# Kernel optimization log

Measured on AMD Instinct MI355X. Metric: run time of the kernel, lower is better.

Reference implementation:

```python
import jax, jax.numpy as jnp
import numpy as np

B, T, D, V, S = 32, 512, 1024, 50257, 16
FWD_SLOTS, NUM_PAIRS, REV_SLOTS, CONF = 4, 4, 2, 0.8
LN_EPS = 1e-5


def setup_inputs() -> dict:
    key = jax.random.key(0)
    ks = jax.random.split(key, 8)
    s = 0.02
    return dict(
        seq=jax.random.randint(ks[0], (B, T), 0, V),
        embed=jax.random.normal(ks[1], (V, D), jnp.float32) * s,
        ff_w1=jax.random.normal(ks[2], (D, 2 * D), jnp.float32) * s,
        ff_b1=jnp.zeros((2 * D,), jnp.float32),
        ff_w2=jax.random.normal(ks[3], (2 * D, D), jnp.float32) * s,
        ff_b2=jnp.zeros((D,), jnp.float32),
        ln_g=jnp.ones((D,), jnp.float32),
        ln_b=jnp.zeros((D,), jnp.float32),
        wg_w=jax.random.normal(ks[4], (D, S), jnp.float32) * s,
        wg_b=jnp.zeros((S,), jnp.float32),
        rp_w=jax.random.normal(ks[5], (D, D), jnp.float32) * s,
        rp_b=jnp.zeros((D,), jnp.float32),
        out_w=jax.random.normal(ks[6], (D, V), jnp.float32) * s,
        out_b=jnp.zeros((V,), jnp.float32),
        memory=jax.random.normal(ks[7], (1, S, D), jnp.float32) * s,
    )


def reference(seq, embed, ff_w1, ff_b1, ff_w2, ff_b2, ln_g, ln_b,
              wg_w, wg_b, rp_w, rp_b, out_w, out_b, memory):
    # --- Encoder: embed -> LayerNorm(h + FFN(h)) ---
    h = embed[seq]                                           # [B,T,D]
    ff = jax.nn.relu(h @ ff_w1 + ff_b1) @ ff_w2 + ff_b2
    x = h + ff
    mu = x.mean(-1, keepdims=True)
    var = ((x - mu) ** 2).mean(-1, keepdims=True)
    hiddens = (x - mu) / jnp.sqrt(var + LN_EPS) * ln_g + ln_b

    # --- write_memory on hiddens[:, :-1, :] ---
    hw = hiddens[:, :-1, :]                                  # [B,Tw,D]
    Tw = hw.shape[1]
    slot_imp = (hw @ wg_w + wg_b).mean(-1)                   # [B,Tw]
    F_size = min(FWD_SLOTS, Tw)
    _, top_idx = jax.lax.top_k(slot_imp, F_size)             # [B,F]
    fwd_hidden = jnp.take_along_axis(hw, top_idx[..., None], axis=1)  # [B,F,D]
    mem = jnp.broadcast_to(memory, (hw.shape[0], S, hw.shape[2]))
    mem = mem.at[:, jnp.arange(F_size) % S].set(fwd_hidden)

    # retroactive writes: skipped = first min(Tw, 2*NUM_PAIRS) positions not in top_idx.
    # Since Kp - F_size >= 4 >= REV_SLOTS, n_rev is always REV_SLOTS (vectorizable).
    Kp = min(Tw, 2 * NUM_PAIRS)
    pos = jnp.arange(Kp)
    in_top = (pos[None, :, None] == top_idx[:, None, :]).any(-1)     # [B,Kp]
    masked = jnp.where(in_top, -jnp.inf, slot_imp[:, :Kp])
    _, rev_pos = jax.lax.top_k(masked, REV_SLOTS)                    # [B,2]
    rev_hidden = jnp.take_along_axis(hw, rev_pos[..., None], axis=1) # [B,2,D]
    mem = mem.at[:, (FWD_SLOTS + jnp.arange(REV_SLOTS)) % S].set(rev_hidden)

    # --- read with suppression ---
    query = hiddens[:, -1, :]                                # [B,D]
    direct_logits = query @ out_w + out_b                    # [B,V]
    conf = jax.nn.softmax(direct_logits, axis=-1).max(-1)
    use_mem = (conf < CONF).astype(query.dtype)[:, None]
    q = query @ rp_w + rp_b
    scores = jnp.einsum('bsd,bd->bs', mem, q)                # [B,S]
    attn = jax.nn.softmax(scores, axis=-1)
    ctx = jnp.einsum('bs,bsd->bd', attn, mem)
    ctx = ctx * use_mem + query * (1.0 - use_mem)
    return ctx @ out_w + out_b                               # [B,V]
```

## Files before the change

kernel.cpp:

```cpp
#include <hip/hip_runtime.h>
#include <stdint.h>
#include <math.h>

#define B_ 32
#define T_ 512
#define D_ 1024
#define H_ 2048
#define V_ 50257
#define S_ 16
#define M_ (B_*T_)
#define TW_ 511

typedef __attribute__((ext_vector_type(8))) short bf16x8;
typedef __attribute__((ext_vector_type(4))) float f32x4;
typedef __attribute__((ext_vector_type(8))) unsigned short us8;
typedef __attribute__((ext_vector_type(4))) unsigned short us4;

__device__ inline unsigned short f2bf(float f) {
  uint32_t u = __builtin_bit_cast(uint32_t, f);
  uint32_t r = (u + 0x7FFFu + ((u >> 16) & 1u)) >> 16;
  return (unsigned short)r;
}
__device__ inline float bf2f(unsigned short h) {
  uint32_t u = ((uint32_t)h) << 16;
  return __builtin_bit_cast(float, u);
}

__device__ inline f32x4 mfma_bf16(bf16x8 a, bf16x8 b, f32x4 c) {
  return __builtin_amdgcn_mfma_f32_16x16x32_bf16(a, b, c, 0, 0, 0);
}

__device__ inline void gl2lds(const unsigned short* g, unsigned short* l) {
  __builtin_amdgcn_global_load_lds(
      (const __attribute__((address_space(1))) unsigned int*)g,
      (__attribute__((address_space(3))) unsigned int*)l,
      16, 0, 0);
}

__global__ __launch_bounds__(256) void k_prep(
    const float* __restrict__ wg_w, const float* __restrict__ wg_b,
    const float* __restrict__ ln_g, const float* __restrict__ ln_b,
    const float* __restrict__ b2,
    float* __restrict__ gu, float* __restrict__ scal) {
  __shared__ float r1[4], r2[4], r3[4], r4[4];
  int tid = threadIdx.x;
  float psgu = 0.f, plbu = 0.f, pb2g = 0.f, pb2s = 0.f;
  for (int d = tid; d < D_; d += 256) {
    float s = 0.f;
    #pragma unroll
    for (int j = 0; j < S_; j++) s += wg_w[d*S_ + j];
    float uu = s * (1.0f/S_);
    float g = ln_g[d] * uu;
    gu[d] = g;
    psgu += g;
    plbu += ln_b[d] * uu;
    pb2g += b2[d] * g;
    pb2s += b2[d];
  }
  for (int off = 32; off > 0; off >>= 1) {
    psgu += __shfl_down(psgu, off, 64); plbu += __shfl_down(plbu, off, 64);
    pb2g += __shfl_down(pb2g, off, 64); pb2s += __shfl_down(pb2s, off, 64);
  }
  if ((tid & 63) == 0) { int w = tid>>6; r1[w]=psgu; r2[w]=plbu; r3[w]=pb2g; r4[w]=pb2s; }
  __syncthreads();
  if (tid == 0) {
    float sgu = r1[0]+r1[1]+r1[2]+r1[3];
    float lbu = r2[0]+r2[1]+r2[2]+r2[3];
    float ub = 0.f;
    for (int j = 0; j < S_; j++) ub += wg_b[j];
    scal[0] = sgu;
    scal[1] = lbu + ub * (1.0f/S_);
    scal[2] = r3[0]+r3[1]+r3[2]+r3[3];
    scal[3] = r4[0]+r4[1]+r4[2]+r4[3];
  }
}

__global__ __launch_bounds__(256) void k_prep2(
    const float* __restrict__ W2, const float* __restrict__ gu,
    float* __restrict__ w2gu, float* __restrict__ w2s) {
  int h = blockIdx.x*4 + (threadIdx.x >> 6);
  int lane = threadIdx.x & 63;
  const float4* row = (const float4*)(W2 + (size_t)h*D_);
  const float4* g4 = (const float4*)gu;
  float sg = 0.f, ss = 0.f;
  #pragma unroll
  for (int k = 0; k < 4; k++) {
    float4 w = row[lane + k*64];
    float4 g = g4[lane + k*64];
    sg += w.x*g.x + w.y*g.y + w.z*g.z + w.w*g.w;
    ss += w.x + w.y + w.z + w.w;
  }
  for (int off = 32; off > 0; off >>= 1) { sg += __shfl_down(sg, off, 64); ss += __shfl_down(ss, off, 64); }
  if (lane == 0) { w2gu[h] = sg; w2s[h] = ss; }
}

__global__ __launch_bounds__(256) void k_gsplit(
    const int* __restrict__ seq, const float* __restrict__ embed,
    const float* __restrict__ gu,
    unsigned short* __restrict__ ehi, unsigned short* __restrict__ elo,
    float* __restrict__ es, float* __restrict__ egu) {
  int m = blockIdx.x;
  int tok = seq[m];
  int tid = threadIdx.x;
  int d = tid * 4;
  float4 v = *(const float4*)(embed + (size_t)tok*D_ + d);
  float4 g = *(const float4*)(gu + d);
  unsigned short h0=f2bf(v.x), h1=f2bf(v.y), h2=f2bf(v.z), h3=f2bf(v.w);
  us4 hv = {h0,h1,h2,h3};
  us4 lv = {f2bf(v.x-bf2f(h0)), f2bf(v.y-bf2f(h1)), f2bf(v.z-bf2f(h2)), f2bf(v.w-bf2f(h3))};
  *(us4*)(ehi + (size_t)m*D_ + d) = hv;
  *(us4*)(elo + (size_t)m*D_ + d) = lv;
  float pe = v.x + v.y + v.z + v.w;
  float pg = v.x*g.x + v.y*g.y + v.z*g.z + v.w*g.w;
  __shared__ float le[4], lg[4];
  for (int off = 32; off > 0; off >>= 1) { pe += __shfl_down(pe, off, 64); pg += __shfl_down(pg, off, 64); }
  if ((tid & 63) == 0) { le[tid>>6] = pe; lg[tid>>6] = pg; }
  __syncthreads();
  if (tid == 0) {
    es[m]  = le[0]+le[1]+le[2]+le[3];
    egu[m] = lg[0]+lg[1]+lg[2]+lg[3];
  }
}

__global__ __launch_bounds__(256) void k_tsplit(
    const float* __restrict__ W, unsigned short* __restrict__ Thi,
    unsigned short* __restrict__ Tlo, int K, int N) {
  __shared__ float tile[32][33];
  int k0 = blockIdx.x * 32, n0 = blockIdx.y * 32;
  int tx = threadIdx.x & 31, ty = threadIdx.x >> 5;
  for (int i = ty; i < 32; i += 8)
    tile[i][tx] = W[(size_t)(k0+i)*N + n0 + tx];
  __syncthreads();
  for (int i = ty; i < 32; i += 8) {
    float v = tile[tx][i];
    unsigned short hi = f2bf(v);
    size_t o = (size_t)(n0+i)*K + k0 + tx;
    Thi[o] = hi;
    if (Tlo) Tlo[o] = f2bf(v - bf2f(hi));
  }
}

__global__ __launch_bounds__(256) void k_gemm1(
    const unsigned short* __restrict__ ehi, const unsigned short* __restrict__ elo,
    const unsigned short* __restrict__ Bhi, const unsigned short* __restrict__ Blo,
    const float* __restrict__ b1,
    const float* __restrict__ w2gu, const float* __restrict__ w2s,
    unsigned short* __restrict__ rhi,
    float* __restrict__ rg, float* __restrict__ rsum) {
  __shared__ unsigned short Ah[128*32], Al[128*32], Bh[128*32], Bl[128*32];
  int m0 = blockIdx.x * 128, n0 = blockIdx.y * 128;
  int tid = threadIdx.x;
  int lane = tid & 63, wave = tid >> 6;
  int wm = (wave & 1) * 64, wn = (wave >> 1) * 64;
  int fr = lane & 15, fq = lane >> 4;
  int srow = lane >> 2;
  int scol = ((lane & 3) ^ ((lane >> 3) & 3)) * 8;
  int csw = (fq ^ ((fr >> 1) & 3)) * 8;

  f32x4 acc[4][4];
  #pragma unroll
  for (int i=0;i<4;i++)
    #pragma unroll
    for (int j=0;j<4;j++) acc[i][j] = (f32x4){0.f,0.f,0.f,0.f};

  const unsigned short *pAh[2], *pAl[2], *pBh[2], *pBl[2];
  unsigned short *lAh[2], *lAl[2], *lBh[2], *lBl[2];
  #pragma unroll
  for (int t = 0; t < 2; t++) {
    int rb = t*64 + wave*16;
    pAh[t] = ehi + (size_t)(m0 + rb + srow)*D_ + scol;
    pAl[t] = elo + (size_t)(m0 + rb + srow)*D_ + scol;
    pBh[t] = Bhi + (size_t)(n0 + rb + srow)*D_ + scol;
    pBl[t] = Blo + (size_t)(n0 + rb + srow)*D_ + scol;
    lAh[t] = &Ah[rb*32]; lAl[t] = &Al[rb*32];
    lBh[t] = &Bh[rb*32]; lBl[t] = &Bl[rb*32];
  }

  for (int k0 = 0; k0 < D_; k0 += 32) {
    #pragma unroll
    for (int t = 0; t < 2; t++) {
      gl2lds(pAh[t], lAh[t]); gl2lds(pAl[t], lAl[t]);
      gl2lds(pBh[t], lBh[t]); gl2lds(pBl[t], lBl[t]);
      pAh[t] += 32; pAl[t] += 32; pBh[t] += 32; pBl[t] += 32;
    }
    __syncthreads();

    bf16x8 ah[4], al[4], bh[4], bl[4];
    #pragma unroll
    for (int i=0;i<4;i++) {
      ah[i] = *(const bf16x8*)&Ah[(wm + i*16 + fr)*32 + csw];
      al[i] = *(const bf16x8*)&Al[(wm + i*16 + fr)*32 + csw];
      bh[i] = *(const bf16x8*)&Bh[(wn + i*16 + fr)*32 + csw];
      bl[i] = *(const bf16x8*)&Bl[(wn + i*16 + fr)*32 + csw];
    }
    #pragma unroll
    for (int i=0;i<4;i++)
      #pragma unroll
      for (int j=0;j<4;j++) {
        acc[i][j] = mfma_bf16(ah[i], bh[j], acc[i][j]);
        acc[i][j] = mfma_bf16(ah[i], bl[j], acc[i][j]);
        acc[i][j] = mfma_bf16(al[i], bh[j], acc[i][j]);
      }
    __syncthreads();
  }

  float biasj[4], wgj[4], wsj[4];
  int gcj[4];
  #pragma unroll
  for (int j=0;j<4;j++) {
    gcj[j] = n0 + wn + j*16 + fr;
    biasj[j] = b1[gcj[j]];
    wgj[j] = w2gu[gcj[j]];
    wsj[j] = w2s[gcj[j]];
  }
  #pragma unroll
  for (int i=0;i<4;i++) {
    #pragma unroll
    for (int r=0;r<4;r++) {
      int gr = m0 + wm + i*16 + fq*4 + r;
      float sg = 0.f, ss = 0.f;
      #pragma unroll
      for (int j=0;j<4;j++) {
        float v = acc[i][j][r] + biasj[j];
        v = fmaxf(v, 0.f);
        rhi[(size_t)gr*H_ + gcj[j]] = f2bf(v);
        sg += v * wgj[j];
        ss += v * wsj[j];
      }
      #pragma unroll
      for (int off = 8; off > 0; off >>= 1) {
        sg += __shfl_down(sg, off, 16);
        ss += __shfl_down(ss, off, 16);
      }
      if (fr == 0) {
        atomicAdd(&rg[gr], sg);
        atomicAdd(&rsum[gr], ss);
      }
    }
  }
}

__global__ __launch_bounds__(256) void k_gemm2(
    const unsigned short* __restrict__ Ahi, const unsigned short* __restrict__ Bhig,
    const float* __restrict__ b2, const int* __restrict__ seq,
    const float* __restrict__ embed, float* __restrict__ xout) {
  __shared__ unsigned short Ah[128*32], Bh[128*32];
  int m0 = blockIdx.x * 128, n0 = blockIdx.y * 128;
  int tid = threadIdx.x;
  int lane = tid & 63, wave = tid >> 6;
  int wm = (wave & 1) * 64, wn = (wave >> 1) * 64;
  int fr = lane & 15, fq = lane >> 4;
  int srow = lane >> 2;
  int scol = ((lane & 3) ^ ((lane >> 3) & 3)) * 8;
  int csw = (fq ^ ((fr >> 1) & 3)) * 8;

  f32x4 acc[4][4];
  #pragma unroll
  for (int i=0;i<4;i++)
    #pragma unroll
    for (int j=0;j<4;j++) acc[i][j] = (f32x4){0.f,0.f,0.f,0.f};

  const unsigned short *pA[2], *pB[2];
  unsigned short *lA[2], *lB[2];
  #pragma unroll
  for (int t = 0; t < 2; t++) {
    int rb = t*64 + wave*16;
    pA[t] = Ahi  + (size_t)(m0 + rb + srow)*H_ + scol;
    pB[t] = Bhig + (size_t)(n0 + rb + srow)*H_ + scol;
    lA[t] = &Ah[rb*32]; lB[t] = &Bh[rb*32];
  }

  for (int k0 = 0; k0 < H_; k0 += 32) {
    #pragma unroll
    for (int t = 0; t < 2; t++) {
      gl2lds(pA[t], lA[t]); gl2lds(pB[t], lB[t]);
      pA[t] += 32; pB[t] += 32;
    }
    __syncthreads();

    bf16x8 ah[4], bh[4];
    #pragma unroll
    for (int i=0;i<4;i++) {
      ah[i] = *(const bf16x8*)&Ah[(wm + i*16 + fr)*32 + csw];
      bh[i] = *(const bf16x8*)&Bh[(wn + i*16 + fr)*32 + csw];
    }
    #pragma unroll
    for (int i=0;i<4;i++)
      #pragma unroll
      for (int j=0;j<4;j++)
        acc[i][j] = mfma_bf16(ah[i], bh[j], acc[i][j]);
    __syncthreads();
  }

  #pragma unroll
  for (int j=0;j<4;j++) {
    int gc = n0 + wn + j*16 + fr;
    float bias = b2[gc];
    #pragma unroll
    for (int i=0;i<4;i++) {
      #pragma unroll
      for (int r=0;r<4;r++) {
        int gr = m0 + wm + i*16 + fq*4 + r;
        float h = embed[(size_t)seq[gr]*D_ + gc];
        xout[(size_t)gr*D_ + gc] = acc[i][j][r] + bias + h;
      }
    }
  }
}

__global__ __launch_bounds__(256) void k_stats(
    const float* __restrict__ x, const float* __restrict__ scal,
    const float* __restrict__ es, const float* __restrict__ egu,
    const float* __restrict__ rg, const float* __restrict__ rsum,
    float* __restrict__ meanv, float* __restrict__ rstdv, float* __restrict__ slotv) {
  int m = blockIdx.x, tid = threadIdx.x;
  const float4* xr = (const float4*)(x + (size_t)m*D_);
  float4 v = xr[tid];
  float sq = v.x*v.x + v.y*v.y + v.z*v.z + v.w*v.w;
  __shared__ float lq[4];
  for (int off = 32; off > 0; off >>= 1) sq += __shfl_down(sq, off, 64);
  if ((tid & 63) == 0) lq[tid>>6] = sq;
  __syncthreads();
  if (tid == 0) {
    sq = lq[0]+lq[1]+lq[2]+lq[3];
    float mu = (es[m] + rsum[m] + scal[3]) * (1.0f/D_);
    float sg = egu[m] + rg[m] + scal[2];
    float var = sq * (1.0f/D_) - mu*mu;
    float rs = 1.0f / sqrtf(var + 1e-5f);
    meanv[m] = mu; rstdv[m] = rs;
    slotv[m] = rs * (sg - mu * scal[0]) + scal[1];
  }
}

__global__ __launch_bounds__(256) void k_select(const float* __restrict__ slotv, int* __restrict__ sel) {
  __shared__ float v[TW_];
  __shared__ float bvs[4]; __shared__ int bis[4];
  int b = blockIdx.x, tid = threadIdx.x;
  for (int t = tid; t < TW_; t += 256) v[t] = slotv[(size_t)b*T_ + t];
  __syncthreads();
  for (int k = 0; k < 4; k++) {
    float bv = -3.4e38f; int bi = 0x7fffffff;
    for (int t = tid; t < TW_; t += 256) {
      float x = v[t];
      if (x > bv) { bv = x; bi = t; }
    }
    for (int off = 32; off > 0; off >>= 1) {
      float ov = __shfl_down(bv, off, 64); int oi = __shfl_down(bi, off, 64);
      if (ov > bv || (ov == bv && oi < bi)) { bv = ov; bi = oi; }
    }
    if ((tid & 63) == 0) { bvs[tid>>6] = bv; bis[tid>>6] = bi; }
    __syncthreads();
    if (tid == 0) {
      float fbv = bvs[0]; int fbi = bis[0];
      for (int w = 1; w < 4; w++)
        if (bvs[w] > fbv || (bvs[w] == fbv && bis[w] < fbi)) { fbv = bvs[w]; fbi = bis[w]; }
      sel[b*8 + k] = fbi; v[fbi] = -3.4e38f;
    }
    __syncthreads();
  }
  if (tid == 0) {
    for (int k = 4; k < 6; k++) {
      float best = -3.4e38f; int bi = 0;
      for (int t = 0; t < 8; t++) if (v[t] > best) { best = v[t]; bi = t; }
      sel[b*8 + k] = bi; v[bi] = -3.4e38f;
    }
  }
}

__global__ __launch_bounds__(256) void k_buildmem(
    const float* __restrict__ x, const float* __restrict__ meanv, const float* __restrict__ rstdv,
    const float* __restrict__ ln_g, const float* __restrict__ ln_b,
    const float* __restrict__ memory, const int* __restrict__ sel,
    float* __restrict__ mem, float* __restrict__ qv) {
  int s = blockIdx.x, b = blockIdx.y, tid = threadIdx.x;
  int d = tid * 4;
  if (s >= 6 && s < 16) {
    *(float4*)&mem[((size_t)b*S_ + s)*D_ + d] = *(const float4*)&memory[(size_t)s*D_ + d];
    return;
  }
  int t = (s == 16) ? (T_ - 1) : sel[b*8 + s];
  int m = b*T_ + t;
  float mu = meanv[m], rs = rstdv[m];
  float4 xv = *(const float4*)&x[(size_t)m*D_ + d];
  float4 g  = *(const float4*)&ln_g[d];
  float4 lb = *(const float4*)&ln_b[d];
  float4 o;
  o.x = (xv.x - mu)*rs*g.x + lb.x;
  o.y = (xv.y - mu)*rs*g.y + lb.y;
  o.z = (xv.z - mu)*rs*g.z + lb.z;
  o.w = (xv.w - mu)*rs*g.w + lb.w;
  if (s == 16) *(float4*)&qv[(size_t)b*D_ + d] = o;
  else         *(float4*)&mem[((size_t)b*S_ + s)*D_ + d] = o;
}

__global__ __launch_bounds__(256) void k_qproj(
    const float* __restrict__ qv, const float* __restrict__ rp_w, const float* __restrict__ rp_b,
    float* __restrict__ q) {
  int j = blockIdx.x * 256 + threadIdx.x;
  int bg = blockIdx.y * 8;
  float acc[8] = {0,0,0,0,0,0,0,0};
  for (int d = 0; d < D_; d++) {
    float w = rp_w[(size_t)d*D_ + j];
    #pragma unroll
    for (int i = 0; i < 8; i++) acc[i] += qv[(size_t)(bg+i)*D_ + d] * w;
  }
  float bias = rp_b[j];
  #pragma unroll
  for (int i = 0; i < 8; i++) q[(size_t)(bg+i)*D_ + j] = acc[i] + bias;
}

__global__ __launch_bounds__(256) void k_attn(
    const float* __restrict__ mem, const float* __restrict__ q,
    float* __restrict__ cm) {
  int b = blockIdx.x, tid = threadIdx.x;
  __shared__ float attnw[S_];
  const float* mb = mem + (size_t)b*S_*D_;
  const float* qb = q + (size_t)b*D_;
  int s = tid >> 4, l = tid & 15;
  float p = 0.f;
  for (int d = l; d < D_; d += 16) p += mb[(size_t)s*D_ + d] * qb[d];
  p += __shfl_down(p, 8, 16);
  p += __shfl_down(p, 4, 16);
  p += __shfl_down(p, 2, 16);
  p += __shfl_down(p, 1, 16);
  if (l == 0) attnw[s] = p;
  __syncthreads();
  if (tid == 0) {
    float mx = attnw[0];
    for (int i = 1; i < S_; i++) mx = fmaxf(mx, attnw[i]);
    float se = 0.f, e[S_];
    for (int i = 0; i < S_; i++) { e[i] = expf(attnw[i] - mx); se += e[i]; }
    for (int i = 0; i < S_; i++) attnw[i] = e[i] / se;
  }
  __syncthreads();
  int d = tid * 4;
  float4 o = {0.f, 0.f, 0.f, 0.f};
  for (int si = 0; si < S_; si++) {
    float a = attnw[si];
    float4 mv = *(const float4*)&mb[(size_t)si*D_ + d];
    o.x += a*mv.x; o.y += a*mv.y; o.z += a*mv.z; o.w += a*mv.w;
  }
  *(float4*)&cm[(size_t)b*D_ + d] = o;
}

__global__ __launch_bounds__(256) void k_tqc(
    const float* __restrict__ qv, const float* __restrict__ cm,
    float* __restrict__ qvT, float* __restrict__ cmT) {
  int i = blockIdx.x*256 + threadIdx.x;
  int d = i >> 5, b = i & 31;
  qvT[i] = qv[(size_t)b*D_ + d];
  cmT[i] = cm[(size_t)b*D_ + d];
}

__global__ __launch_bounds__(256) void k_logits(
    const float* __restrict__ qvT, const float* __restrict__ cmT,
    const float* __restrict__ out_w,
    float* __restrict__ pdl, float* __restrict__ pcl) {
  int v = blockIdx.x*256 + threadIdx.x;
  if (v >= V_) return;
  int bg = (blockIdx.y & 1) * 16;
  int dc = blockIdx.y >> 1;
  int d0 = dc * 512, d1 = d0 + 512;
  float4 aq[4], ac[4];
  #pragma unroll
  for (int i = 0; i < 4; i++) { aq[i] = (float4){0,0,0,0}; ac[i] = (float4){0,0,0,0}; }
  for (int d = d0; d < d1; d++) {
    float w = out_w[(size_t)d*V_ + v];
    const float4* qt = (const float4*)(qvT + d*32 + bg);
    const float4* ct = (const float4*)(cmT + d*32 + bg);
    #pragma unroll
    for (int i = 0; i < 4; i++) {
      float4 qq = qt[i], cc = ct[i];
      aq[i].x += qq.x*w; aq[i].y += qq.y*w; aq[i].z += qq.z*w; aq[i].w += qq.w*w;
      ac[i].x += cc.x*w; ac[i].y += cc.y*w; ac[i].z += cc.z*w; ac[i].w += cc.w*w;
    }
  }
  size_t cb = (size_t)dc * 32;
  #pragma unroll
  for (int i = 0; i < 4; i++) {
    pdl[(cb + bg + i*4 + 0)*V_ + v] = aq[i].x;
    pdl[(cb + bg + i*4 + 1)*V_ + v] = aq[i].y;
    pdl[(cb + bg + i*4 + 2)*V_ + v] = aq[i].z;
    pdl[(cb + bg + i*4 + 3)*V_ + v] = aq[i].w;
    pcl[(cb + bg + i*4 + 0)*V_ + v] = ac[i].x;
    pcl[(cb + bg + i*4 + 1)*V_ + v] = ac[i].y;
    pcl[(cb + bg + i*4 + 2)*V_ + v] = ac[i].z;
    pcl[(cb + bg + i*4 + 3)*V_ + v] = ac[i].w;
  }
}

__global__ __launch_bounds__(256) void k_lreduce(
    const float* __restrict__ pdl, const float* __restrict__ pcl,
    const float* __restrict__ out_b,
    float* __restrict__ dl, float* __restrict__ cl) {
  int v = blockIdx.x*256 + threadIdx.x;
  if (v >= V_) return;
  int b = blockIdx.y;
  float ob = out_b[v];
  size_t o = (size_t)b*V_ + v;
  size_t o2 = (size_t)(b+32)*V_ + v;
  dl[o] = pdl[o] + pdl[o2] + ob;
  cl[o] = pcl[o] + pcl[o2] + ob;
}

__global__ __launch_bounds__(256) void k_conf(const float* __restrict__ dl, float* __restrict__ um) {
  int b = blockIdx.x, tid = threadIdx.x;
  __shared__ float red[4];
  const float* row = dl + (size_t)b*V_;
  float mx = -3.4e38f;
  for (int v = tid; v < V_; v += 256) mx = fmaxf(mx, row[v]);
  for (int off = 32; off > 0; off >>= 1) mx = fmaxf(mx, __shfl_down(mx, off, 64));
  if ((tid & 63) == 0) red[tid>>6] = mx;
  __syncthreads();
  mx = fmaxf(fmaxf(red[0], red[1]), fmaxf(red[2], red[3]));
  __syncthreads();
  float s = 0.f;
  for (int v = tid; v < V_; v += 256) s += expf(row[v] - mx);
  for (int off = 32; off > 0; off >>= 1) s += __shfl_down(s, off, 64);
  if ((tid & 63) == 0) red[tid>>6] = s;
  __syncthreads();
  if (tid == 0) {
    s = red[0]+red[1]+red[2]+red[3];
    float conf = 1.0f / s;
    um[b] = (conf < 0.8f) ? 1.0f : 0.0f;
  }
}

__global__ __launch_bounds__(256) void k_out(
    const float* __restrict__ dl, const float* __restrict__ cl,
    const float* __restrict__ um, float* __restrict__ out) {
  int i = blockIdx.x*256 + threadIdx.x;
  if (i >= B_*V_) return;
  int b = i / V_;
  out[i] = (um[b] > 0.5f) ? cl[i] : dl[i];
}

extern "C" void kernel_launch(void* const* d_in, const int* in_sizes, int n_in,
                              void* d_out, int out_size, void* d_ws, size_t ws_size,
                              hipStream_t stream) {
  const int*   seq    = (const int*)d_in[0];
  const float* embed  = (const float*)d_in[1];
  const float* ff_w1  = (const float*)d_in[2];
  const float* ff_b1  = (const float*)d_in[3];
  const float* ff_w2  = (const float*)d_in[4];
  const float* ff_b2  = (const float*)d_in[5];
  const float* ln_g   = (const float*)d_in[6];
  const float* ln_b   = (const float*)d_in[7];
  const float* wg_w   = (const float*)d_in[8];
  const float* wg_b   = (const float*)d_in[9];
  const float* rp_w   = (const float*)d_in[10];
  const float* rp_b   = (const float*)d_in[11];
  const float* out_w  = (const float*)d_in[12];
  const float* out_b  = (const float*)d_in[13];
  const float* memory = (const float*)d_in[14];
  float* out = (float*)d_out;

  char* p = (char*)d_ws;
  auto alloc = [&](size_t bytes) { char* r = p; p += (bytes + 255) & ~(size_t)255; return r; };

  unsigned short* w1thi = (unsigned short*)alloc((size_t)H_*D_*2);
  unsigned short* w1tlo = (unsigned short*)alloc((size_t)H_*D_*2);
  unsigned short* w2thi = (unsigned short*)alloc((size_t)D_*H_*2);
  unsigned short* rhi   = (unsigned short*)alloc((size_t)M_*H_*2);
  unsigned short* ehi   = (unsigned short*)alloc((size_t)M_*D_*2);
  unsigned short* elo   = (unsigned short*)alloc((size_t)M_*D_*2);
  float* xbuf  = (float*)ehi;
  float* gu    = (float*)alloc((size_t)D_*4);
  float* scal  = (float*)alloc(256);
  float* w2gu  = (float*)alloc((size_t)H_*4);
  float* w2s   = (float*)alloc((size_t)H_*4);
  float* es    = (float*)alloc((size_t)M_*4);
  float* egu   = (float*)alloc((size_t)M_*4);
  float* rg    = (float*)alloc((size_t)M_*4);
  float* rsum  = (float*)alloc((size_t)M_*4);
  float* meanv = (float*)alloc((size_t)M_*4);
  float* rstdv = (float*)alloc((size_t)M_*4);
  float* slotv = (float*)alloc((size_t)M_*4);
  int*   sel   = (int*)alloc((size_t)B_*8*4);
  float* memb  = (float*)alloc((size_t)B_*S_*D_*4);
  float* qv    = (float*)alloc((size_t)B_*D_*4);
  float* qproj = (float*)alloc((size_t)B_*D_*4);
  float* cm    = (float*)alloc((size_t)B_*D_*4);
  float* qvT   = (float*)alloc((size_t)B_*D_*4);
  float* cmT   = (float*)alloc((size_t)B_*D_*4);
  float* dl    = (float*)alloc((size_t)B_*V_*4);
  float* cl    = (float*)alloc((size_t)B_*V_*4);
  float* pdl   = (float*)alloc((size_t)64*V_*4);
  float* pcl   = (float*)alloc((size_t)64*V_*4);
  float* um    = (float*)alloc((size_t)B_*4);

  hipMemsetAsync(rg,   0, (size_t)M_*4, stream);
  hipMemsetAsync(rsum, 0, (size_t)M_*4, stream);
  hipLaunchKernelGGL(k_prep, dim3(1), dim3(256), 0, stream, wg_w, wg_b, ln_g, ln_b, ff_b2, gu, scal);
  hipLaunchKernelGGL(k_prep2, dim3(H_/4), dim3(256), 0, stream, ff_w2, gu, w2gu, w2s);
  hipLaunchKernelGGL(k_gsplit, dim3(M_), dim3(256), 0, stream, seq, embed, gu, ehi, elo, es, egu);
  hipLaunchKernelGGL(k_tsplit, dim3(D_/32, H_/32), dim3(256), 0, stream, ff_w1, w1thi, w1tlo, D_, H_);
  hipLaunchKernelGGL(k_tsplit, dim3(H_/32, D_/32), dim3(256), 0, stream, ff_w2, w2thi, (unsigned short*)nullptr, H_, D_);
  hipLaunchKernelGGL(k_gemm1, dim3(M_/128, H_/128), dim3(256), 0, stream,
                     ehi, elo, w1thi, w1tlo, ff_b1, w2gu, w2s, rhi, rg, rsum);
  hipLaunchKernelGGL(k_gemm2, dim3(M_/128, D_/128), dim3(256), 0, stream,
                     rhi, w2thi, ff_b2, seq, embed, xbuf);
  hipLaunchKernelGGL(k_stats, dim3(M_), dim3(256), 0, stream, xbuf, scal, es, egu, rg, rsum,
                     meanv, rstdv, slotv);
  hipLaunchKernelGGL(k_select, dim3(B_), dim3(256), 0, stream, slotv, sel);
  hipLaunchKernelGGL(k_buildmem, dim3(17, B_), dim3(256), 0, stream,
                     xbuf, meanv, rstdv, ln_g, ln_b, memory, sel, memb, qv);
  hipLaunchKernelGGL(k_qproj, dim3(D_/256, 4), dim3(256), 0, stream, qv, rp_w, rp_b, qproj);
  hipLaunchKernelGGL(k_attn, dim3(B_), dim3(256), 0, stream, memb, qproj, cm);
  hipLaunchKernelGGL(k_tqc, dim3((D_*B_)/256), dim3(256), 0, stream, qv, cm, qvT, cmT);
  hipLaunchKernelGGL(k_logits, dim3((V_+255)/256, 4), dim3(256), 0, stream,
                     qvT, cmT, out_w, pdl, pcl);
  hipLaunchKernelGGL(k_lreduce, dim3((V_+255)/256, 32), dim3(256), 0, stream,
                     pdl, pcl, out_b, dl, cl);
  hipLaunchKernelGGL(k_conf, dim3(B_), dim3(256), 0, stream, dl, um);
  hipLaunchKernelGGL(k_out, dim3((B_*V_+255)/256), dim3(256), 0, stream, dl, cl, um, out);
}
```

Baseline: 1.171 ms.

## Compute output logits with bf16 MFMA over packed query/context rows

Replaces the scalar FP32 logits kernel, which split D in two and needed a separate partial-sum reduction, with one MFMA-based kernel. The 32 query rows and 32 context rows are packed into a 64-row bf16 matrix, and out_w columns are converted to bf16 in shared memory. Bias is added in the epilogue, so the partial buffers and the reduce kernel go away. This trades FP32 accuracy for bf16 inputs in the final logits, which could change the confidence threshold decision. The grid also drops to about 197 blocks with no D split, which may underuse the GPU.

```diff
diff --git a/kernel.cpp b/kernel.cpp
--- a/kernel.cpp
+++ b/kernel.cpp
@@ -443,64 +443,82 @@
   *(float4*)&cm[(size_t)b*D_ + d] = o;
 }
 
-__global__ __launch_bounds__(256) void k_tqc(
+__global__ __launch_bounds__(256) void k_xpack(
     const float* __restrict__ qv, const float* __restrict__ cm,
-    float* __restrict__ qvT, float* __restrict__ cmT) {
-  int i = blockIdx.x*256 + threadIdx.x;
-  int d = i >> 5, b = i & 31;
-  qvT[i] = qv[(size_t)b*D_ + d];
-  cmT[i] = cm[(size_t)b*D_ + d];
+    unsigned short* __restrict__ x64) {
+  int r = blockIdx.x;
+  const float* src = (r < 32) ? (qv + (size_t)r*D_) : (cm + (size_t)(r-32)*D_);
+  int d = threadIdx.x * 4;
+  float4 v = *(const float4*)(src + d);
+  us4 hv = {f2bf(v.x), f2bf(v.y), f2bf(v.z), f2bf(v.w)};
+  *(us4*)(x64 + (size_t)r*D_ + d) = hv;
 }
 
 __global__ __launch_bounds__(256) void k_logits(
-    const float* __restrict__ qvT, const float* __restrict__ cmT,
-    const float* __restrict__ out_w,
-    float* __restrict__ pdl, float* __restrict__ pcl) {
-  int v = blockIdx.x*256 + threadIdx.x;
-  if (v >= V_) return;
-  int bg = (blockIdx.y & 1) * 16;
-  int dc = blockIdx.y >> 1;
-  int d0 = dc * 512, d1 = d0 + 512;
-  float4 aq[4], ac[4];
-  #pragma unroll
-  for (int i = 0; i < 4; i++) { aq[i] = (float4){0,0,0,0}; ac[i] = (float4){0,0,0,0}; }
-  for (int d = d0; d < d1; d++) {
-    float w = out_w[(size_t)d*V_ + v];
-    const float4* qt = (const float4*)(qvT + d*32 + bg);
-    const float4* ct = (const float4*)(cmT + d*32 + bg);
-    #pragma unroll
-    for (int i = 0; i < 4; i++) {
-      float4 qq = qt[i], cc = ct[i];
-      aq[i].x += qq.x*w; aq[i].y += qq.y*w; aq[i].z += qq.z*w; aq[i].w += qq.w*w;
-      ac[i].x += cc.x*w; ac[i].y += cc.y*w; ac[i].z += cc.z*w; ac[i].w += cc.w*w;
-    }
-  }
-  size_t cb = (size_t)dc * 32;
-  #pragma unroll
-  for (int i = 0; i < 4; i++) {
-    pdl[(cb + bg + i*4 + 0)*V_ + v] = aq[i].x;
-    pdl[(cb + bg + i*4 + 1)*V_ + v] = aq[i].y;
-    pdl[(cb + bg + i*4 + 2)*V_ + v] = aq[i].z;
-    pdl[(cb + bg + i*4 + 3)*V_ + v] = aq[i].w;
-    pcl[(cb + bg + i*4 + 0)*V_ + v] = ac[i].x;
-    pcl[(cb + bg + i*4 + 1)*V_ + v] = ac[i].y;
-    pcl[(cb + bg + i*4 + 2)*V_ + v] = ac[i].z;
-    pcl[(cb + bg + i*4 + 3)*V_ + v] = ac[i].w;
-  }
-}
-
-__global__ __launch_bounds__(256) void k_lreduce(
-    const float* __restrict__ pdl, const float* __restrict__ pcl,
+    const unsigned short* __restrict__ x64, const float* __restrict__ out_w,
     const float* __restrict__ out_b,
     float* __restrict__ dl, float* __restrict__ cl) {
-  int v = blockIdx.x*256 + threadIdx.x;
-  if (v >= V_) return;
-  int b = blockIdx.y;
-  float ob = out_b[v];
-  size_t o = (size_t)b*V_ + v;
-  size_t o2 = (size_t)(b+32)*V_ + v;
-  dl[o] = pdl[o] + pdl[o2] + ob;
-  cl[o] = pcl[o] + pcl[o2] + ob;
+  __shared__ unsigned short Bs[32*256];
+  int n0 = blockIdx.x * 256;
+  int tid = threadIdx.x;
+  int lane = tid & 63, wave = tid >> 6;
+  int wn = wave * 64;
+  int fr = lane & 15, fq = lane >> 4;
+
+  bool colok = (n0 + tid) < V_;
+  const float* gcol = out_w + (size_t)0*V_ + n0 + tid;
+
+  f32x4 acc[4][4];
+  #pragma unroll
+  for (int i=0;i<4;i++)
+    #pragma unroll
+    for (int j=0;j<4;j++) acc[i][j] = (f32x4){0.f,0.f,0.f,0.f};
+
+  for (int k0 = 0; k0 < D_; k0 += 32) {
+    #pragma unroll
+    for (int k = 0; k < 32; k++) {
+      float v = colok ? gcol[(size_t)(k0+k)*V_] : 0.f;
+      Bs[k*256 + tid] = f2bf(v);
+    }
+    __syncthreads();
+
+    bf16x8 af[4], bf[4];
+    #pragma unroll
+    for (int i=0;i<4;i++)
+      af[i] = *(const bf16x8*)(x64 + (size_t)(i*16+fr)*D_ + k0 + fq*8);
+    #pragma unroll
+    for (int j=0;j<4;j++) {
+      int col = wn + j*16 + fr;
+      unsigned short tmp[8];
+      #pragma unroll
+      for (int r8=0;r8<8;r8++) tmp[r8] = Bs[(fq*8+r8)*256 + col];
+      bf[j] = *(const bf16x8*)tmp;
+    }
+    #pragma unroll
+    for (int i=0;i<4;i++)
+      #pragma unroll
+      for (int j=0;j<4;j++)
+        acc[i][j] = mfma_bf16(af[i], bf[j], acc[i][j]);
+    __syncthreads();
+  }
+
+  #pragma unroll
+  for (int j=0;j<4;j++) {
+    int n = n0 + wn + j*16 + fr;
+    if (n < V_) {
+      float ob = out_b[n];
+      #pragma unroll
+      for (int i=0;i<4;i++) {
+        #pragma unroll
+        for (int r=0;r<4;r++) {
+          int row = i*16 + fq*4 + r;
+          float val = acc[i][j][r] + ob;
+          if (row < 32) dl[(size_t)row*V_ + n] = val;
+          else          cl[(size_t)(row-32)*V_ + n] = val;
+        }
+      }
+    }
+  }
 }
 
 __global__ __launch_bounds__(256) void k_conf(const float* __restrict__ dl, float* __restrict__ um) {
@@ -581,12 +599,9 @@
   float* qv    = (float*)alloc((size_t)B_*D_*4);
   float* qproj = (float*)alloc((size_t)B_*D_*4);
   float* cm    = (float*)alloc((size_t)B_*D_*4);
-  float* qvT   = (float*)alloc((size_t)B_*D_*4);
-  float* cmT   = (float*)alloc((size_t)B_*D_*4);
+  unsigned short* x64 = (unsigned short*)alloc((size_t)64*D_*2);
   float* dl    = (float*)alloc((size_t)B_*V_*4);
   float* cl    = (float*)alloc((size_t)B_*V_*4);
-  float* pdl   = (float*)alloc((size_t)64*V_*4);
-  float* pcl   = (float*)alloc((size_t)64*V_*4);
   float* um    = (float*)alloc((size_t)B_*4);
 
   hipMemsetAsync(rg,   0, (size_t)M_*4, stream);
@@ -607,11 +622,9 @@
                      xbuf, meanv, rstdv, ln_g, ln_b, memory, sel, memb, qv);
   hipLaunchKernelGGL(k_qproj, dim3(D_/256, 4), dim3(256), 0, stream, qv, rp_w, rp_b, qproj);
   hipLaunchKernelGGL(k_attn, dim3(B_), dim3(256), 0, stream, memb, qproj, cm);
-  hipLaunchKernelGGL(k_tqc, dim3((D_*B_)/256), dim3(256), 0, stream, qv, cm, qvT, cmT);
-  hipLaunchKernelGGL(k_logits, dim3((V_+255)/256, 4), dim3(256), 0, stream,
-                     qvT, cmT, out_w, pdl, pcl);
-  hipLaunchKernelGGL(k_lreduce, dim3((V_+255)/256, 32), dim3(256), 0, stream,
-                     pdl, pcl, out_b, dl, cl);
+  hipLaunchKernelGGL(k_xpack, dim3(64), dim3(256), 0, stream, qv, cm, x64);
+  hipLaunchKernelGGL(k_logits, dim3((V_+255)/256), dim3(256), 0, stream,
+                     x64, out_w, out_b, dl, cl);
   hipLaunchKernelGGL(k_conf, dim3(B_), dim3(256), 0, stream, dl, um);
   hipLaunchKernelGGL(k_out, dim3((B_*V_+255)/256), dim3(256), 0, stream, dl, cl, um, out);
 }
```

Result: no change. 1.186 ms (+1.3%).
